# Performance work log

Measured on AMD Instinct MI355X. Metric: run time of the kernel, lower is better.

## Reference

```python
import jax, jax.numpy as jnp
import numpy as np
import math

B, S, D, H = 64, 575, 256, 8
FF = 4 * D
EPS = 1e-5
DILATIONS = (1, 2, 4)


def _ln(x, g, b):
    mu = jnp.mean(x, axis=-1, keepdims=True)
    var = jnp.var(x, axis=-1, keepdims=True)
    return (x - mu) * jax.lax.rsqrt(var + EPS) * g + b


def setup_inputs() -> dict:
    key = jax.random.key(0)
    ks = jax.random.split(key, 8)
    w = lambda k, shape: jax.random.normal(k, shape, jnp.float32) * 0.02
    return {
        'state': jax.random.normal(ks[0], (B, S, D), jnp.float32),
        'conv_w': w(ks[1], (3, D, D, 3, 3)),
        'conv_b': jnp.zeros((3, D), jnp.float32),
        'qkv_w': w(ks[2], (3 * D, D)),
        'qkv_b': jnp.zeros((3 * D,), jnp.float32),
        'o_w': w(ks[3], (D, D)),
        'o_b': jnp.zeros((D,), jnp.float32),
        'attn_bias': w(ks[4], (H, S, S)),
        'ffp_w': w(ks[5], (FF, D)),
        'ffp_b': jnp.zeros((FF,), jnp.float32),
        'ffg_w': w(ks[6], (FF, D)),
        'ffg_b': jnp.zeros((FF,), jnp.float32),
        'ffo_w': w(ks[7], (D, FF)),
        'ffo_b': jnp.zeros((D,), jnp.float32),
        'n1_g': jnp.ones((D,), jnp.float32), 'n1_b': jnp.zeros((D,), jnp.float32),
        'n2_g': jnp.ones((D,), jnp.float32), 'n2_b': jnp.zeros((D,), jnp.float32),
        'n3_g': jnp.ones((D,), jnp.float32), 'n3_b': jnp.zeros((D,), jnp.float32),
    }


def _forward(state, conv_w, conv_b, qkv_w, qkv_b, o_w, o_b, attn_bias,
             ffp_w, ffp_b, ffg_w, ffg_b, ffo_w, ffo_b,
             n1_g, n1_b, n2_g, n2_b, n3_g, n3_b):
    b, s, d = state.shape
    h = attn_bias.shape[0]
    hd = d // h
    spatial = int(round(math.sqrt(s + 1)))  # grid_size + 1; spatial^2 == s+1 here

    # --- multi-scale dilated conv mixing ---
    pad = jnp.zeros((b, 1, d), state.dtype)
    h2d = jnp.concatenate([pad, state], axis=1)            # (B, S+1, D)
    h2d = jnp.transpose(h2d, (0, 2, 1)).reshape(b, d, spatial, spatial)
    conv_sum = 0.0
    for i, dil in enumerate(DILATIONS):
        y = jax.lax.conv_general_dilated(
            h2d, conv_w[i], window_strides=(1, 1),
            padding=[(dil, dil), (dil, dil)], rhs_dilation=(dil, dil),
            dimension_numbers=('NCHW', 'OIHW', 'NCHW'))
        conv_sum = conv_sum + y + conv_b[i][None, :, None, None]
    h_flat = jnp.transpose(conv_sum.reshape(b, d, -1), (0, 2, 1))  # (B, S+1, D)
    hmix = h_flat[:, 1:, :]

    state = _ln(state + hmix, n1_g, n1_b)

    # --- self-attention with learned per-head pair bias ---
    qkv = state @ qkv_w.T + qkv_b                          # (B, S, 3D)
    q, k, v = jnp.split(qkv, 3, axis=-1)
    # NOTE: replicate torch's reshape (no transpose): (B,S,D) -> (B,H,S,hd)
    q = q.reshape(b, h, s, hd)
    k = k.reshape(b, h, s, hd)
    v = v.reshape(b, h, s, hd)
    scores = jnp.einsum('bhsd,bhtd->bhst', q, k) / math.sqrt(hd)
    scores = scores + attn_bias[None]
    attn = jax.nn.softmax(scores, axis=-1)
    out = jnp.einsum('bhst,bhtd->bhsd', attn, v)
    out = jnp.transpose(out, (0, 2, 1, 3)).reshape(b, s, d)

    state = _ln(state + out @ o_w.T + o_b, n2_g, n2_b)

    # --- gated feed-forward ---
    proj = state @ ffp_w.T + ffp_b
    gate = jax.nn.sigmoid(state @ ffg_w.T + ffg_b)
    ff = (proj * gate) @ ffo_w.T + ffo_b
    return _ln(state + ff, n3_g, n3_b)


def reference(state, conv_w, conv_b, qkv_w, qkv_b, o_w, o_b, attn_bias,
              ffp_w, ffp_b, ffg_w, ffg_b, ffo_w, ffo_b,
              n1_g, n1_b, n2_g, n2_b, n3_g, n3_b):
    return _forward(state, conv_w, conv_b, qkv_w, qkv_b, o_w, o_b, attn_bias,
                    ffp_w, ffp_b, ffg_w, ffg_b, ffo_w, ffo_b,
                    n1_g, n1_b, n2_g, n2_b, n3_g, n3_b)
```

## Files before the change

kernel.cpp:

```cpp
#include <hip/hip_runtime.h>
#include <hip/hip_bf16.h>
#include <cstdio>


typedef __attribute__((ext_vector_type(8))) short s8v;
typedef __attribute__((ext_vector_type(4))) float f32x4;
typedef unsigned short u16;

constexpr int kB = 64, kS = 575, kD = 256, kH = 8, kP = 576, kFF = 1024;
constexpr int kRows = kB * kS;
constexpr float kEps = 1e-5f;
constexpr float kScale = 0.17677669529663687f;
constexpr size_t kPdStride = 9420800;

__device__ __forceinline__ u16 f2b(float f) {
  __hip_bfloat16 h = __float2bfloat16(f);
  return *reinterpret_cast<u16*>(&h);
}
__device__ __forceinline__ void unpack2(unsigned int w, float& lo, float& hi) {
  union { float f; unsigned int u; } a, b;
  a.u = w << 16;
  b.u = w & 0xffff0000u;
  lo = a.f;
  hi = b.f;
}

__device__ __forceinline__ void gll16(const void* g, void* l) {
  __builtin_amdgcn_global_load_lds((const __attribute__((address_space(1))) void*)g,
                                   (__attribute__((address_space(3))) void*)l, 16, 0, 0);
}

__global__ void k_pack_convw(const float* __restrict__ cw, u16* __restrict__ wc) {
  int idx = blockIdx.x * 256 + threadIdx.x;
  if (idx >= 27 * kD * kD) return;
  int ci = idx & 255;
  int co = (idx >> 8) & 255;
  int tap = idx >> 16;
  int i = tap / 9, r = tap - i * 9;
  int ky = r / 3, kx = r - ky * 3;
  wc[idx] = f2b(cw[(((size_t)(i * kD + co) * kD + ci) * 3 + ky) * 3 + kx]);
}

__global__ void k_tobf16(const float* __restrict__ in, u16* __restrict__ out, int n) {
  int i = blockIdx.x * 256 + threadIdx.x;
  if (i < n) out[i] = f2b(in[i]);
}

__global__ void k_make_x0(const float* __restrict__ state, u16* __restrict__ x0,
                          u16* __restrict__ zrow) {
  int bp = blockIdx.x;
  int c = threadIdx.x;
  if (bp == kB * kP) { zrow[c] = 0; return; }
  int p = bp % kP;
  int b = bp / kP;
  float v = (p == 0) ? 0.f : state[((size_t)(b * kS + p - 1)) * kD + c];
  x0[(size_t)bp * kD + c] = f2b(v);
}

__global__ __launch_bounds__(256) void k_gemm(const u16* __restrict__ A,
                                              const u16* __restrict__ Bw,
                                              const float* __restrict__ bias,
                                              u16* __restrict__ Cb,
                                              int M, int N, int K) {
  __shared__ u16 As[8192];
  __shared__ u16 Bs[8192];
  const int t = threadIdx.x;
  const int wave = t >> 6, lane = t & 63;
  const int wm = wave >> 1, wn = wave & 1;
  const int lr = lane & 15, lk = lane >> 4;
  const int m0 = blockIdx.x * 128, n0 = blockIdx.y * 128;
  const int lrow = lane >> 3;
  const int swzk = ((lane & 7) ^ lrow) * 8;
  int arow[4], brow[4];
#pragma unroll
  for (int i = 0; i < 4; ++i) {
    int r = 8 * wave + lrow + 32 * i;
    int ra = m0 + r;
    if (ra > M - 1) ra = M - 1;
    arow[i] = ra;
    brow[i] = n0 + r;
  }
  f32x4 acc[4][4] = {};
  for (int kt = 0; kt < K; kt += 64) {
#pragma unroll
    for (int i = 0; i < 4; ++i) {
      gll16(A + (size_t)arow[i] * K + kt + swzk, As + i * 2048 + wave * 512);
      gll16(Bw + (size_t)brow[i] * K + kt + swzk, Bs + i * 2048 + wave * 512);
    }
    __syncthreads();
    s8v af[2][4], bfr[2][4];
#pragma unroll
    for (int kk = 0; kk < 2; ++kk)
#pragma unroll
      for (int i = 0; i < 4; ++i) {
        const int rA = wm * 64 + i * 16 + lr;
        const int rB = wn * 64 + i * 16 + lr;
        af[kk][i] = *(const s8v*)(As + rA * 64 + ((kk * 32 + lk * 8) ^ ((rA & 7) << 3)));
        bfr[kk][i] = *(const s8v*)(Bs + rB * 64 + ((kk * 32 + lk * 8) ^ ((rB & 7) << 3)));
      }
#pragma unroll
    for (int kk = 0; kk < 2; ++kk)
#pragma unroll
      for (int i = 0; i < 4; ++i)
#pragma unroll
        for (int j = 0; j < 4; ++j)
          acc[i][j] = __builtin_amdgcn_mfma_f32_16x16x32_bf16(af[kk][i], bfr[kk][j], acc[i][j], 0, 0, 0);
    __syncthreads();
  }
#pragma unroll
  for (int i = 0; i < 4; ++i) {
    const int rbase = m0 + wm * 64 + i * 16 + lk * 4;
#pragma unroll
    for (int j = 0; j < 4; ++j) {
      const int col = n0 + wn * 64 + j * 16 + lr;
      const float bv = bias[col];
#pragma unroll
      for (int q = 0; q < 4; ++q) {
        int r = rbase + q;
        if (r < M) Cb[(size_t)r * N + col] = f2b(acc[i][j][q] + bv);
      }
    }
  }
}

__global__ __launch_bounds__(256) void k_ff1(const u16* __restrict__ A,
                                             const u16* __restrict__ Wf,
                                             const float* __restrict__ pb,
                                             const float* __restrict__ gb,
                                             u16* __restrict__ H, int M) {
  __shared__ u16 As[4096];
  __shared__ u16 Bp[4096];
  __shared__ u16 Bg[4096];
  const int t = threadIdx.x;
  const int wave = t >> 6;
  const int wm = wave >> 1, wn = wave & 1;
  const int lr = threadIdx.x & 15, lk = (threadIdx.x & 63) >> 4;
  const int m0 = blockIdx.x * 128, n0 = blockIdx.y * 128;
  int ra = m0 + (t >> 2);
  int rb = ra + 64;
  if (ra > M - 1) ra = M - 1;
  if (rb > M - 1) rb = M - 1;
  const int koff = (t & 3) * 8;
  const u16* gA0 = A + (size_t)ra * kD + koff;
  const u16* gA1 = A + (size_t)rb * kD + koff;
  const u16* gP0 = Wf + (size_t)(n0 + (t >> 2)) * kD + koff;
  const u16* gP1 = gP0 + (size_t)64 * kD;
  const u16* gG0 = gP0 + (size_t)1024 * kD;
  const u16* gG1 = gP1 + (size_t)1024 * kD;
  u16* lA0 = As + wave * 512;
  u16* lA1 = As + 2048 + wave * 512;
  u16* lP0 = Bp + wave * 512;
  u16* lP1 = Bp + 2048 + wave * 512;
  u16* lG0 = Bg + wave * 512;
  u16* lG1 = Bg + 2048 + wave * 512;
  f32x4 ap[4][4] = {};
  f32x4 ag[4][4] = {};
  for (int kt = 0; kt < kD; kt += 32) {
    gll16(gA0 + kt, lA0);
    gll16(gA1 + kt, lA1);
    gll16(gP0 + kt, lP0);
    gll16(gP1 + kt, lP1);
    gll16(gG0 + kt, lG0);
    gll16(gG1 + kt, lG1);
    __syncthreads();
    s8v af[4], bp4[4], bg4[4];
#pragma unroll
    for (int i = 0; i < 4; ++i) {
      af[i] = *(const s8v*)(As + (wm * 64 + i * 16 + lr) * 32 + lk * 8);
      bp4[i] = *(const s8v*)(Bp + (wn * 64 + i * 16 + lr) * 32 + lk * 8);
      bg4[i] = *(const s8v*)(Bg + (wn * 64 + i * 16 + lr) * 32 + lk * 8);
    }
#pragma unroll
    for (int i = 0; i < 4; ++i)
#pragma unroll
      for (int j = 0; j < 4; ++j) {
        ap[i][j] = __builtin_amdgcn_mfma_f32_16x16x32_bf16(af[i], bp4[j], ap[i][j], 0, 0, 0);
        ag[i][j] = __builtin_amdgcn_mfma_f32_16x16x32_bf16(af[i], bg4[j], ag[i][j], 0, 0, 0);
      }
    __syncthreads();
  }
#pragma unroll
  for (int i = 0; i < 4; ++i) {
    const int rbase = m0 + wm * 64 + i * 16 + lk * 4;
#pragma unroll
    for (int j = 0; j < 4; ++j) {
      const int col = n0 + wn * 64 + j * 16 + lr;
      const float pbv = pb[col], gbv = gb[col];
#pragma unroll
      for (int q = 0; q < 4; ++q) {
        int r = rbase + q;
        if (r < M) {
          float p = ap[i][j][q] + pbv;
          float g = ag[i][j][q] + gbv;
          H[(size_t)r * kFF + col] = f2b(p * (1.f / (1.f + __expf(-g))));
        }
      }
    }
  }
}

__global__ __launch_bounds__(256) void k_conv(const u16* __restrict__ X0,
                                              const u16* __restrict__ zrow,
                                              const u16* __restrict__ Wc,
                                              const float* __restrict__ cb,
                                              u16* __restrict__ pd) {
  __shared__ u16 As[8192];
  __shared__ u16 Bs[8192];
  const int t = threadIdx.x;
  const int wave = t >> 6, lane = t & 63;
  const int wm = wave >> 1, wn = wave & 1;
  const int lr = lane & 15, lk = lane >> 4;
  const int m0 = blockIdx.x * 128;
  const int di = blockIdx.y >> 1;
  const int n0 = (blockIdx.y & 1) * 128;
  const int b = blockIdx.z;
  const int dil = 1 << di;
  const int lrow = lane >> 3;
  const int swzk = ((lane & 7) ^ lrow) * 8;
  int prow[4], py[4], px[4], wrow[4];
#pragma unroll
  for (int i = 0; i < 4; ++i) {
    int r = 8 * wave + lrow + 32 * i;
    prow[i] = m0 + r;
    py[i] = prow[i] / 24;
    px[i] = prow[i] - py[i] * 24;
    wrow[i] = n0 + r;
  }
  const u16* Wd = Wc + (size_t)di * 9 * kD * kD;
  u16* pdo = pd + (size_t)di * kPdStride;
  f32x4 acc[4][4] = {};
  for (int rtap = 0; rtap < 9; ++rtap) {
    const int dy = (rtap / 3 - 1) * dil;
    const int dx = (rtap % 3 - 1) * dil;
    const u16* src[4];
#pragma unroll
    for (int i = 0; i < 4; ++i) {
      const int ny = py[i] + dy, nx = px[i] + dx;
      const bool v = (prow[i] < 576) && ((unsigned)ny < 24u) && ((unsigned)nx < 24u);
      src[i] = v ? X0 + ((size_t)(b * kP + ny * 24 + nx)) * kD + swzk : zrow + swzk;
    }
    const u16* wB = Wd + (size_t)rtap * (kD * kD);
    for (int kc = 0; kc < kD; kc += 64) {
#pragma unroll
      for (int i = 0; i < 4; ++i) {
        gll16(src[i] + kc, As + i * 2048 + wave * 512);
        gll16(wB + (size_t)wrow[i] * kD + kc + swzk, Bs + i * 2048 + wave * 512);
      }
      __syncthreads();
      s8v af[2][4], bfr[2][4];
#pragma unroll
      for (int kk = 0; kk < 2; ++kk)
#pragma unroll
        for (int ii = 0; ii < 4; ++ii) {
          const int rA = wm * 64 + ii * 16 + lr;
          const int rB = wn * 64 + ii * 16 + lr;
          af[kk][ii] = *(const s8v*)(As + rA * 64 + ((kk * 32 + lk * 8) ^ ((rA & 7) << 3)));
          bfr[kk][ii] = *(const s8v*)(Bs + rB * 64 + ((kk * 32 + lk * 8) ^ ((rB & 7) << 3)));
        }
#pragma unroll
      for (int kk = 0; kk < 2; ++kk)
#pragma unroll
        for (int ii = 0; ii < 4; ++ii)
#pragma unroll
          for (int jj = 0; jj < 4; ++jj)
            acc[ii][jj] = __builtin_amdgcn_mfma_f32_16x16x32_bf16(af[kk][ii], bfr[kk][jj], acc[ii][jj], 0, 0, 0);
      __syncthreads();
    }
  }
#pragma unroll
  for (int i2 = 0; i2 < 4; ++i2) {
    const int pbase = m0 + wm * 64 + i2 * 16 + lk * 4;
#pragma unroll
    for (int j = 0; j < 4; ++j) {
      const int col = n0 + wn * 64 + j * 16 + lr;
      const float bv = cb[di * kD + col];
#pragma unroll
      for (int q = 0; q < 4; ++q) {
        int p = pbase + q;
        if (p >= 1 && p < 576)
          pdo[((size_t)(b * kS + p - 1)) * kD + col] = f2b(acc[i2][j][q] + bv);
      }
    }
  }
}

__global__ __launch_bounds__(256) void k_attn2(const u16* __restrict__ qkv,
                                               const float* __restrict__ bias,
                                               u16* __restrict__ outp) {
  __shared__ u16 KsS[2][2048];
  __shared__ u16 VtS[2][2048];
  __shared__ u16 PsS[4][1024];
  const int qt = blockIdx.x, h = blockIdx.y, b = blockIdx.z;
  const int tid = threadIdx.x;
  const int w = tid >> 6, lane = tid & 63;
  const int lg = lane >> 4, lr = lane & 15;
  const int q0 = qt * 64;
  const int qrow_a = q0 + w * 16 + lr;
  const int qrow_ac = qrow_a < kS ? qrow_a : kS - 1;
  s8v qf;
  {
    int F = h * (kS * 32) + qrow_ac * 32 + lg * 8;
    qf = *(const s8v*)(qkv + ((size_t)(b * kS + (F >> 8))) * 768 + (F & 255));
  }
  const int trel = tid >> 2;
  const int dcol = (tid & 3) * 8;
  float mrun[4], lsum[4];
#pragma unroll
  for (int r = 0; r < 4; ++r) { mrun[r] = -1e30f; lsum[r] = 0.f; }
  f32x4 o0 = {0.f, 0.f, 0.f, 0.f}, o1 = {0.f, 0.f, 0.f, 0.f};
  const f32x4 zf = {0.f, 0.f, 0.f, 0.f};
  const int qrow_s = q0 + w * 16 + lg * 4;
  const size_t kvrowbase = (size_t)(b * kS) * 768;

  for (int kt = 0; kt < 9; ++kt) {
    const int t0 = kt * 64;
    const int buf = kt & 1;
    {
      const int tg = t0 + trel;
      const bool tv = tg < kS;
      const int tcl = tv ? tg : kS - 1;
      const int Fk = h * (kS * 32) + tcl * 32 + dcol;
      const u16* kp = qkv + kvrowbase + (size_t)(Fk >> 8) * 768 + 256 + (Fk & 255);
      uint4 kd = {0, 0, 0, 0}, vd = {0, 0, 0, 0};
      if (tv) {
        kd = *(const uint4*)kp;
        vd = *(const uint4*)(kp + 256);
      }
      *(uint4*)&KsS[buf][trel * 32 + (dcol ^ ((trel & 3) << 3))] = kd;
      union { uint4 u4; u16 us[8]; } vu;
      vu.u4 = vd;
#pragma unroll
      for (int j = 0; j < 8; ++j) {
        const int d = dcol + j;
        VtS[buf][d * 64 + (trel ^ ((d & 7) << 3))] = vu.us[j];
      }
    }
    float bv[4][4];
#pragma unroll
    for (int r = 0; r < 4; ++r) {
      const int qr = qrow_s + r;
      const float* bp = bias + ((size_t)h * kS + (qr < kS ? qr : kS - 1)) * kS;
#pragma unroll
      for (int j = 0; j < 4; ++j) {
        const int tg = t0 + j * 16 + lr;
        bv[j][r] = (tg < kS) ? bp[tg] : -1e30f;
      }
    }
    __syncthreads();
    f32x4 sc[4];
#pragma unroll
    for (int j = 0; j < 4; ++j) {
      const int krow = j * 16 + lr;
      s8v kf = *(const s8v*)&KsS[buf][krow * 32 + ((lg * 8) ^ ((krow & 3) << 3))];
      sc[j] = __builtin_amdgcn_mfma_f32_16x16x32_bf16(qf, kf, zf, 0, 0, 0);
    }
#pragma unroll
    for (int r = 0; r < 4; ++r) {
      float s4[4];
      float sm = -1e30f;
#pragma unroll
      for (int j = 0; j < 4; ++j) {
        s4[j] = fmaf(sc[j][r], kScale, bv[j][r]);
        sm = fmaxf(sm, s4[j]);
      }
      sm = fmaxf(sm, __shfl_xor(sm, 1));
      sm = fmaxf(sm, __shfl_xor(sm, 2));
      sm = fmaxf(sm, __shfl_xor(sm, 4));
      sm = fmaxf(sm, __shfl_xor(sm, 8));
      const float nm = fmaxf(mrun[r], sm);
      const float corr = __expf(mrun[r] - nm);
      mrun[r] = nm;
      float psum = 0.f;
      const int prow = lg * 4 + r;
#pragma unroll
      for (int j = 0; j < 4; ++j) {
        const float p = __expf(s4[j] - nm);
        psum += p;
        PsS[w][prow * 64 + ((j * 16 + lr) ^ ((prow & 7) << 3))] = f2b(p);
      }
      lsum[r] = fmaf(lsum[r], corr, psum);
      o0[r] *= corr;
      o1[r] *= corr;
    }
#pragma unroll
    for (int c = 0; c < 2; ++c) {
      const int pcol = c * 32 + lg * 8;
      s8v pf = *(const s8v*)&PsS[w][lr * 64 + (pcol ^ ((lr & 7) << 3))];
      s8v vf0 = *(const s8v*)&VtS[buf][lr * 64 + (pcol ^ ((lr & 7) << 3))];
      s8v vf1 = *(const s8v*)&VtS[buf][(16 + lr) * 64 + (pcol ^ (((16 + lr) & 7) << 3))];
      o0 = __builtin_amdgcn_mfma_f32_16x16x32_bf16(pf, vf0, o0, 0, 0, 0);
      o1 = __builtin_amdgcn_mfma_f32_16x16x32_bf16(pf, vf1, o1, 0, 0, 0);
    }
  }
#pragma unroll
  for (int r = 0; r < 4; ++r) {
    float lt = lsum[r];
    lt += __shfl_xor(lt, 1);
    lt += __shfl_xor(lt, 2);
    lt += __shfl_xor(lt, 4);
    lt += __shfl_xor(lt, 8);
    const float inv = 1.f / lt;
    const int qr = qrow_s + r;
    if (qr < kS) {
      u16* op = outp + ((size_t)(b * kS + qr)) * kD + h * 32;
      op[lr] = f2b(o0[r] * inv);
      op[16 + lr] = f2b(o1[r] * inv);
    }
  }
}

__global__ __launch_bounds__(256) void k_add_ln(const float* __restrict__ xa,
                                                const u16* __restrict__ xb,
                                                const float* __restrict__ g,
                                                const float* __restrict__ be,
                                                float* __restrict__ of, u16* __restrict__ ob) {
  const int wave = threadIdx.x >> 6, lane = threadIdx.x & 63;
  const int row = blockIdx.x * 4 + wave;
  const float4 a = ((const float4*)(xa + (size_t)row * kD))[lane];
  uint2 bw = ((const uint2*)(xb + (size_t)row * kD))[lane];
  float b0, b1, b2, b3;
  unpack2(bw.x, b0, b1);
  unpack2(bw.y, b2, b3);
  float x0 = a.x + b0, x1 = a.y + b1, x2 = a.z + b2, x3 = a.w + b3;
  float sum = x0 + x1 + x2 + x3;
  float sq = fmaf(x0, x0, fmaf(x1, x1, fmaf(x2, x2, x3 * x3)));
  for (int off = 1; off < 64; off <<= 1) {
    sum += __shfl_xor(sum, off);
    sq += __shfl_xor(sq, off);
  }
  const float mean = sum * (1.f / 256.f);
  const float var = sq * (1.f / 256.f) - mean * mean;
  const float rs = rsqrtf(var + kEps);
  const float4 gg = ((const float4*)g)[lane];
  const float4 bt = ((const float4*)be)[lane];
  float y0 = (x0 - mean) * rs * gg.x + bt.x;
  float y1 = (x1 - mean) * rs * gg.y + bt.y;
  float y2 = (x2 - mean) * rs * gg.z + bt.z;
  float y3 = (x3 - mean) * rs * gg.w + bt.w;
  float4 yo = {y0, y1, y2, y3};
  ((float4*)(of + (size_t)row * kD))[lane] = yo;
  if (ob) {
    u16* po = ob + (size_t)row * kD + lane * 4;
    po[0] = f2b(y0); po[1] = f2b(y1); po[2] = f2b(y2); po[3] = f2b(y3);
  }
}

__global__ __launch_bounds__(256) void k_add_ln3(const float* __restrict__ xa,
                                                 const u16* __restrict__ pa,
                                                 const u16* __restrict__ pbq,
                                                 const u16* __restrict__ pc,
                                                 const float* __restrict__ g,
                                                 const float* __restrict__ be,
                                                 float* __restrict__ of, u16* __restrict__ ob) {
  const int wave = threadIdx.x >> 6, lane = threadIdx.x & 63;
  const int row = blockIdx.x * 4 + wave;
  const size_t base = (size_t)row * kD;
  const float4 a = ((const float4*)(xa + base))[lane];
  uint2 w0 = ((const uint2*)(pa + base))[lane];
  uint2 w1 = ((const uint2*)(pbq + base))[lane];
  uint2 w2 = ((const uint2*)(pc + base))[lane];
  float a0, a1, a2, a3, c0, c1, c2, c3, d0, d1, d2, d3;
  unpack2(w0.x, a0, a1); unpack2(w0.y, a2, a3);
  unpack2(w1.x, c0, c1); unpack2(w1.y, c2, c3);
  unpack2(w2.x, d0, d1); unpack2(w2.y, d2, d3);
  float x0 = a.x + a0 + c0 + d0, x1 = a.y + a1 + c1 + d1;
  float x2 = a.z + a2 + c2 + d2, x3 = a.w + a3 + c3 + d3;
  float sum = x0 + x1 + x2 + x3;
  float sq = fmaf(x0, x0, fmaf(x1, x1, fmaf(x2, x2, x3 * x3)));
  for (int off = 1; off < 64; off <<= 1) {
    sum += __shfl_xor(sum, off);
    sq += __shfl_xor(sq, off);
  }
  const float mean = sum * (1.f / 256.f);
  const float var = sq * (1.f / 256.f) - mean * mean;
  const float rs = rsqrtf(var + kEps);
  const float4 gg = ((const float4*)g)[lane];
  const float4 bt = ((const float4*)be)[lane];
  float y0 = (x0 - mean) * rs * gg.x + bt.x;
  float y1 = (x1 - mean) * rs * gg.y + bt.y;
  float y2 = (x2 - mean) * rs * gg.z + bt.z;
  float y3 = (x3 - mean) * rs * gg.w + bt.w;
  float4 yo = {y0, y1, y2, y3};
  ((float4*)(of + base))[lane] = yo;
  u16* po = ob + base + lane * 4;
  po[0] = f2b(y0); po[1] = f2b(y1); po[2] = f2b(y2); po[3] = f2b(y3);
}

extern "C" void kernel_launch(void* const* d_in, const int* in_sizes, int n_in,
                              void* d_out, int out_size, void* d_ws, size_t ws_size,
                              hipStream_t stream) {
  const float* state = (const float*)d_in[0];
  const float* conv_w = (const float*)d_in[1];
  const float* conv_b = (const float*)d_in[2];
  const float* qkv_w = (const float*)d_in[3];
  const float* qkv_b = (const float*)d_in[4];
  const float* o_w = (const float*)d_in[5];
  const float* o_b = (const float*)d_in[6];
  const float* attn_bias = (const float*)d_in[7];
  const float* ffp_w = (const float*)d_in[8];
  const float* ffp_b = (const float*)d_in[9];
  const float* ffg_w = (const float*)d_in[10];
  const float* ffg_b = (const float*)d_in[11];
  const float* ffo_w = (const float*)d_in[12];
  const float* ffo_b = (const float*)d_in[13];
  const float* n1_g = (const float*)d_in[14];
  const float* n1_b = (const float*)d_in[15];
  const float* n2_g = (const float*)d_in[16];
  const float* n2_b = (const float*)d_in[17];
  const float* n3_g = (const float*)d_in[18];
  const float* n3_b = (const float*)d_in[19];

  constexpr size_t kWsNeed = 137527296;
  if (ws_size < kWsNeed) {
    fprintf(stderr, "[kernel] ws_size=%zu < need=%zu\n", ws_size, kWsNeed);
    return;
  }
  char* ws = (char*)d_ws;
  u16* Wc = (u16*)(ws + 0);
  u16* Wqkv = (u16*)(ws + 3538944);
  u16* Wo = (u16*)(ws + 3932160);
  u16* Wff = (u16*)(ws + 4063232);
  u16* Wffo = (u16*)(ws + 5111808);
  float* stF = (float*)(ws + 5636096);
  u16* stB = (u16*)(ws + 43319296);
  char* S4 = ws + 62160896;
  u16* X0 = (u16*)(ws + 5636096);
  u16* zrow = (u16*)(ws + 43319296);
  u16* pd = (u16*)S4;
  u16* qkvb = (u16*)S4;
  u16* attnout = (u16*)(S4 + 56524800);
  u16* oprojb = (u16*)S4;
  u16* ffh = (u16*)S4;
  float* outp = (float*)d_out;

  k_pack_convw<<<6912, 256, 0, stream>>>(conv_w, Wc);
  k_tobf16<<<768, 256, 0, stream>>>(qkv_w, Wqkv, 768 * 256);
  k_tobf16<<<256, 256, 0, stream>>>(o_w, Wo, 256 * 256);
  k_tobf16<<<1024, 256, 0, stream>>>(ffp_w, Wff, 1024 * 256);
  k_tobf16<<<1024, 256, 0, stream>>>(ffg_w, Wff + 1024 * 256, 1024 * 256);
  k_tobf16<<<1024, 256, 0, stream>>>(ffo_w, Wffo, 256 * 1024);
  k_make_x0<<<kB * kP + 1, 256, 0, stream>>>(state, X0, zrow);

  k_conv<<<dim3(5, 6, kB), 256, 0, stream>>>(X0, zrow, Wc, conv_b, pd);
  k_add_ln3<<<kRows / 4, 256, 0, stream>>>(state, pd, pd + kPdStride, pd + 2 * kPdStride,
                                           n1_g, n1_b, stF, stB);

  k_gemm<<<dim3(288, 6), 256, 0, stream>>>(stB, Wqkv, qkv_b, qkvb, kRows, 768, 256);
  k_attn2<<<dim3(9, kH, kB), 256, 0, stream>>>(qkvb, attn_bias, attnout);
  k_gemm<<<dim3(288, 2), 256, 0, stream>>>(attnout, Wo, o_b, oprojb, kRows, 256, 256);
  k_add_ln<<<kRows / 4, 256, 0, stream>>>(stF, oprojb, n2_g, n2_b, stF, stB);

  k_ff1<<<dim3(288, 8), 256, 0, stream>>>(stB, Wff, ffp_b, ffg_b, ffh, kRows);
  k_gemm<<<dim3(288, 2), 256, 0, stream>>>(ffh, Wffo, ffo_b, stB, kRows, 256, 1024);
  k_add_ln<<<kRows / 4, 256, 0, stream>>>(stF, stB, n3_g, n3_b, outp, nullptr);
}
```

Baseline: 620.4 us.

## Double-buffer LDS in GEMM and conv kernels; flatten conv M across batch

Adds two-stage LDS double buffering to the generic GEMM and the implicit-GEMM conv kernel, so the next K-tile's global-to-LDS loads are issued before the current tile's MFMAs and one barrier per iteration is dropped. The conv kernel also stops tiling each 576-position image separately: it flattens batch×positions into one M dimension (64·576 rows, divisible by 128) and regrids so padded tail tiles are no longer wasted. This doubles LDS use to 64KB per block, which may reduce occupancy.

```diff
diff --git a/kernel.cpp b/kernel.cpp
--- a/kernel.cpp
+++ b/kernel.cpp
@@ -62,8 +62,8 @@
                                               const float* __restrict__ bias,
                                               u16* __restrict__ Cb,
                                               int M, int N, int K) {
-  __shared__ u16 As[8192];
-  __shared__ u16 Bs[8192];
+  __shared__ u16 As[2][8192];
+  __shared__ u16 Bs[2][8192];
   const int t = threadIdx.x;
   const int wave = t >> 6, lane = t & 63;
   const int wm = wave >> 1, wn = wave & 1;
@@ -71,23 +71,29 @@
   const int m0 = blockIdx.x * 128, n0 = blockIdx.y * 128;
   const int lrow = lane >> 3;
   const int swzk = ((lane & 7) ^ lrow) * 8;
-  int arow[4], brow[4];
+  const u16 *ga[4], *gb[4];
 #pragma unroll
   for (int i = 0; i < 4; ++i) {
     int r = 8 * wave + lrow + 32 * i;
     int ra = m0 + r;
     if (ra > M - 1) ra = M - 1;
-    arow[i] = ra;
-    brow[i] = n0 + r;
-  }
+    ga[i] = A + (size_t)ra * K + swzk;
+    gb[i] = Bw + (size_t)(n0 + r) * K + swzk;
+  }
+  auto stage = [&](int kt, int buf) {
+#pragma unroll
+    for (int i = 0; i < 4; ++i) {
+      gll16(ga[i] + kt, &As[buf][i * 2048 + wave * 512]);
+      gll16(gb[i] + kt, &Bs[buf][i * 2048 + wave * 512]);
+    }
+  };
   f32x4 acc[4][4] = {};
-  for (int kt = 0; kt < K; kt += 64) {
-#pragma unroll
-    for (int i = 0; i < 4; ++i) {
-      gll16(A + (size_t)arow[i] * K + kt + swzk, As + i * 2048 + wave * 512);
-      gll16(Bw + (size_t)brow[i] * K + kt + swzk, Bs + i * 2048 + wave * 512);
-    }
-    __syncthreads();
+  stage(0, 0);
+  __syncthreads();
+  const int NT = K >> 6;
+  for (int s = 0; s < NT; ++s) {
+    const int cur = s & 1;
+    if (s + 1 < NT) stage((s + 1) << 6, cur ^ 1);
     s8v af[2][4], bfr[2][4];
 #pragma unroll
     for (int kk = 0; kk < 2; ++kk)
@@ -95,8 +101,8 @@
       for (int i = 0; i < 4; ++i) {
         const int rA = wm * 64 + i * 16 + lr;
         const int rB = wn * 64 + i * 16 + lr;
-        af[kk][i] = *(const s8v*)(As + rA * 64 + ((kk * 32 + lk * 8) ^ ((rA & 7) << 3)));
-        bfr[kk][i] = *(const s8v*)(Bs + rB * 64 + ((kk * 32 + lk * 8) ^ ((rB & 7) << 3)));
+        af[kk][i] = *(const s8v*)(&As[cur][rA * 64 + ((kk * 32 + lk * 8) ^ ((rA & 7) << 3))]);
+        bfr[kk][i] = *(const s8v*)(&Bs[cur][rB * 64 + ((kk * 32 + lk * 8) ^ ((rB & 7) << 3))]);
       }
 #pragma unroll
     for (int kk = 0; kk < 2; ++kk)
@@ -204,81 +210,85 @@
                                               const u16* __restrict__ Wc,
                                               const float* __restrict__ cb,
                                               u16* __restrict__ pd) {
-  __shared__ u16 As[8192];
-  __shared__ u16 Bs[8192];
+  __shared__ u16 As[2][8192];
+  __shared__ u16 Bs[2][8192];
   const int t = threadIdx.x;
   const int wave = t >> 6, lane = t & 63;
   const int wm = wave >> 1, wn = wave & 1;
   const int lr = lane & 15, lk = lane >> 4;
   const int m0 = blockIdx.x * 128;
-  const int di = blockIdx.y >> 1;
-  const int n0 = (blockIdx.y & 1) * 128;
-  const int b = blockIdx.z;
+  const int n0 = blockIdx.y * 128;
+  const int di = blockIdx.z;
   const int dil = 1 << di;
   const int lrow = lane >> 3;
   const int swzk = ((lane & 7) ^ lrow) * 8;
-  int prow[4], py[4], px[4], wrow[4];
+  const u16* Wd = Wc + (size_t)di * 9 * (kD * kD);
+  int bb[4], py[4], px[4];
+  const u16* gw[4];
 #pragma unroll
   for (int i = 0; i < 4; ++i) {
     int r = 8 * wave + lrow + 32 * i;
-    prow[i] = m0 + r;
-    py[i] = prow[i] / 24;
-    px[i] = prow[i] - py[i] * 24;
-    wrow[i] = n0 + r;
-  }
-  const u16* Wd = Wc + (size_t)di * 9 * kD * kD;
-  u16* pdo = pd + (size_t)di * kPdStride;
-  f32x4 acc[4][4] = {};
-  for (int rtap = 0; rtap < 9; ++rtap) {
-    const int dy = (rtap / 3 - 1) * dil;
-    const int dx = (rtap % 3 - 1) * dil;
-    const u16* src[4];
+    int m = m0 + r;
+    bb[i] = m / 576;
+    int p = m - bb[i] * 576;
+    py[i] = p / 24;
+    px[i] = p - py[i] * 24;
+    gw[i] = Wd + (size_t)(n0 + r) * kD + swzk;
+  }
+  auto stage = [&](int s, int buf) {
+    const int tap = s >> 2, kc = (s & 3) << 6;
+    const int dy = (tap / 3 - 1) * dil;
+    const int dx = (tap % 3 - 1) * dil;
 #pragma unroll
     for (int i = 0; i < 4; ++i) {
       const int ny = py[i] + dy, nx = px[i] + dx;
-      const bool v = (prow[i] < 576) && ((unsigned)ny < 24u) && ((unsigned)nx < 24u);
-      src[i] = v ? X0 + ((size_t)(b * kP + ny * 24 + nx)) * kD + swzk : zrow + swzk;
-    }
-    const u16* wB = Wd + (size_t)rtap * (kD * kD);
-    for (int kc = 0; kc < kD; kc += 64) {
-#pragma unroll
-      for (int i = 0; i < 4; ++i) {
-        gll16(src[i] + kc, As + i * 2048 + wave * 512);
-        gll16(wB + (size_t)wrow[i] * kD + kc + swzk, Bs + i * 2048 + wave * 512);
-      }
-      __syncthreads();
-      s8v af[2][4], bfr[2][4];
-#pragma unroll
-      for (int kk = 0; kk < 2; ++kk)
-#pragma unroll
-        for (int ii = 0; ii < 4; ++ii) {
-          const int rA = wm * 64 + ii * 16 + lr;
-          const int rB = wn * 64 + ii * 16 + lr;
-          af[kk][ii] = *(const s8v*)(As + rA * 64 + ((kk * 32 + lk * 8) ^ ((rA & 7) << 3)));
-          bfr[kk][ii] = *(const s8v*)(Bs + rB * 64 + ((kk * 32 + lk * 8) ^ ((rB & 7) << 3)));
-        }
-#pragma unroll
-      for (int kk = 0; kk < 2; ++kk)
-#pragma unroll
-        for (int ii = 0; ii < 4; ++ii)
-#pragma unroll
-          for (int jj = 0; jj < 4; ++jj)
-            acc[ii][jj] = __builtin_amdgcn_mfma_f32_16x16x32_bf16(af[kk][ii], bfr[kk][jj], acc[ii][jj], 0, 0, 0);
-      __syncthreads();
-    }
-  }
+      const bool v = ((unsigned)ny < 24u) & ((unsigned)nx < 24u);
+      const u16* sa = v ? X0 + (((size_t)(bb[i] * kP + ny * 24 + nx)) << 8) + kc + swzk
+                        : zrow + swzk;
+      gll16(sa, &As[buf][i * 2048 + wave * 512]);
+      gll16(gw[i] + (size_t)tap * (kD * kD) + kc, &Bs[buf][i * 2048 + wave * 512]);
+    }
+  };
+  f32x4 acc[4][4] = {};
+  stage(0, 0);
+  __syncthreads();
+  for (int s = 0; s < 36; ++s) {
+    const int cur = s & 1;
+    if (s < 35) stage(s + 1, cur ^ 1);
+    s8v af[2][4], bfr[2][4];
+#pragma unroll
+    for (int kk = 0; kk < 2; ++kk)
+#pragma unroll
+      for (int ii = 0; ii < 4; ++ii) {
+        const int rA = wm * 64 + ii * 16 + lr;
+        const int rB = wn * 64 + ii * 16 + lr;
+        af[kk][ii] = *(const s8v*)(&As[cur][rA * 64 + ((kk * 32 + lk * 8) ^ ((rA & 7) << 3))]);
+        bfr[kk][ii] = *(const s8v*)(&Bs[cur][rB * 64 + ((kk * 32 + lk * 8) ^ ((rB & 7) << 3))]);
+      }
+#pragma unroll
+    for (int kk = 0; kk < 2; ++kk)
+#pragma unroll
+      for (int ii = 0; ii < 4; ++ii)
+#pragma unroll
+        for (int jj = 0; jj < 4; ++jj)
+          acc[ii][jj] = __builtin_amdgcn_mfma_f32_16x16x32_bf16(af[kk][ii], bfr[kk][jj], acc[ii][jj], 0, 0, 0);
+    __syncthreads();
+  }
+  u16* pdo = pd + (size_t)di * kPdStride;
 #pragma unroll
   for (int i2 = 0; i2 < 4; ++i2) {
-    const int pbase = m0 + wm * 64 + i2 * 16 + lk * 4;
+    const int mbase = m0 + wm * 64 + i2 * 16 + lk * 4;
 #pragma unroll
     for (int j = 0; j < 4; ++j) {
       const int col = n0 + wn * 64 + j * 16 + lr;
       const float bv = cb[di * kD + col];
 #pragma unroll
       for (int q = 0; q < 4; ++q) {
-        int p = pbase + q;
-        if (p >= 1 && p < 576)
-          pdo[((size_t)(b * kS + p - 1)) * kD + col] = f2b(acc[i2][j][q] + bv);
+        const int m = mbase + q;
+        const int b2 = m / 576;
+        const int p = m - b2 * 576;
+        if (p >= 1)
+          pdo[((size_t)(b2 * kS + p - 1) << 8) + col] = f2b(acc[i2][j][q] + bv);
       }
     }
   }
@@ -541,7 +551,7 @@
   k_tobf16<<<1024, 256, 0, stream>>>(ffo_w, Wffo, 256 * 1024);
   k_make_x0<<<kB * kP + 1, 256, 0, stream>>>(state, X0, zrow);
 
-  k_conv<<<dim3(5, 6, kB), 256, 0, stream>>>(X0, zrow, Wc, conv_b, pd);
+  k_conv<<<dim3(288, 2, 3), 256, 0, stream>>>(X0, zrow, Wc, conv_b, pd);
   k_add_ln3<<<kRows / 4, 256, 0, stream>>>(state, pd, pd + kPdStride, pd + 2 * kPdStride,
                                            n1_g, n1_b, stF, stB);
 
```

New measurement: 612.7 us. Within noise of the previous version (-1.2%).
